# Optimization experiments

Hardware: AMD Instinct MI355X
Metric: run time of the kernel (lower is better)

The kernel has to match this reference:

```python
import jax, jax.numpy as jnp
import numpy as np

B, S, D, H = 2, 2048, 1024, 16
DH = D // H


def setup_inputs() -> dict:
    key = jax.random.key(0)
    ks = jax.random.split(key, 6)
    scale = 0.02
    X = jax.random.normal(ks[0], (B, S, D), dtype=jnp.float32)
    masks = jax.random.randint(ks[1], (B, S), 0, 2).astype(jnp.int32)
    Wq = jax.random.normal(ks[2], (D, D), dtype=jnp.float32) * scale
    Wk = jax.random.normal(ks[3], (D, D), dtype=jnp.float32) * scale
    Wv = jax.random.normal(ks[4], (D, D), dtype=jnp.float32) * scale
    Wo = jax.random.normal(ks[5], (D, D), dtype=jnp.float32) * scale
    return {"X": X, "masks": masks, "Wq": Wq, "Wk": Wk, "Wv": Wv, "Wo": Wo}


def reference(X, masks, Wq, Wk, Wv, Wo):
    b, s, d = X.shape
    masks_b = masks.astype(bool)                       # [B,S] key validity
    lookahead = jnp.triu(jnp.ones((s, s), dtype=bool), 1)  # [S,S] future positions
    pad = ~masks_b[:, None, :]                         # [B,1,S] -> invalid keys
    invalid = pad | lookahead[None, :, :]              # [B,S,S]
    valid = (~invalid)[:, None, :, :].astype(X.dtype)  # [B,1,S,S]

    def split_heads(Y):  # [B,S,D] -> [B,H,S,DH]
        return Y.reshape(b, s, H, DH).transpose(0, 2, 1, 3)

    Q = split_heads(X @ Wq.T)
    K = split_heads(X @ Wk.T)
    V = split_heads(X @ Wv.T)

    Qn = Q / jnp.sqrt(jnp.sum(Q * Q, axis=-1, keepdims=True))
    Kn = K / jnp.sqrt(jnp.sum(K * K, axis=-1, keepdims=True))

    scores = jnp.einsum('bhqd,bhkd->bhqk', Qn, Kn)     # cosine similarities
    att = jax.nn.relu(scores) * valid                  # relu + causal/pad mask
    ctx = jnp.einsum('bhqk,bhkd->bhqd', att, V)
    ctx = ctx * masks_b[:, None, :, None].astype(X.dtype)  # zero padded queries

    out = ctx.transpose(0, 2, 1, 3).reshape(b, s, d)
    return out @ Wo.T
```

## Files before the change

kernel.cpp:

```cpp
#include <hip/hip_runtime.h>
#include <hip/hip_bf16.h>

#define BB 2
#define SS 2048
#define DD 1024
#define HH 16
#define MMR (BB*SS)
#define ND3 3072

typedef __hip_bfloat16 bf;
typedef __bf16 bf16x8 __attribute__((ext_vector_type(8)));
typedef float f32x4 __attribute__((ext_vector_type(4)));
typedef float f32x16 __attribute__((ext_vector_type(16)));

#define VMCNT(n) asm volatile("s_waitcnt vmcnt(" #n ")" ::: "memory")

__device__ __forceinline__ f32x4 mfma16(bf16x8 a, bf16x8 b, f32x4 c) {
    return __builtin_amdgcn_mfma_f32_16x16x32_bf16(a, b, c, 0, 0, 0);
}
__device__ __forceinline__ f32x16 mfma32(bf16x8 a, bf16x8 b, f32x16 c) {
    return __builtin_amdgcn_mfma_f32_32x32x16_bf16(a, b, c, 0, 0, 0);
}
__device__ __forceinline__ unsigned cvt_pk_bf16(float lo, float hi) {
    unsigned r;
    asm("v_cvt_pk_bf16_f32 %0, %1, %2" : "=v"(r) : "v"(lo), "v"(hi));
    return r;
}
__device__ __forceinline__ void pl32swap(unsigned& a, unsigned& b) {
    asm("v_permlane32_swap_b32 %0, %1" : "+v"(a), "+v"(b));
}
__device__ __forceinline__ void glds16(const bf* g, bf* l) {
    __builtin_amdgcn_global_load_lds(
        (const __attribute__((address_space(1))) void*)g,
        (__attribute__((address_space(3))) void*)l,
        16, 0, 0);
}

__global__ __launch_bounds__(256) void k_convert(const float* __restrict__ X,
                                                 const float* __restrict__ Wq,
                                                 const float* __restrict__ Wk,
                                                 const float* __restrict__ Wv,
                                                 const float* __restrict__ Wo,
                                                 bf* __restrict__ Xb,
                                                 bf* __restrict__ Wqkv,
                                                 bf* __restrict__ Wob) {
    const int bid = blockIdx.x;
    const float* src;
    bf* dst;
    int off;
    if (bid < 4096) {
        src = X; dst = Xb; off = bid;
    } else {
        const int r = (bid - 4096) >> 10;
        src = (r == 0) ? Wq : (r == 1) ? Wk : (r == 2) ? Wv : Wo;
        dst = (r < 3) ? (Wqkv + (size_t)r * 1048576) : Wob;
        off = (bid - 4096) & 1023;
    }
    const int j = (off * 256 + threadIdx.x) * 4;
    float4 v = *(const float4*)(src + j);
    bf tmp[4];
    tmp[0] = __float2bfloat16(v.x);
    tmp[1] = __float2bfloat16(v.y);
    tmp[2] = __float2bfloat16(v.z);
    tmp[3] = __float2bfloat16(v.w);
    *(uint2*)(dst + j) = *(const uint2*)tmp;
}

template<int MODE, int BM, int BN>
__global__ __launch_bounds__(256) void k_gemm(const bf* __restrict__ A,
                                              const bf* __restrict__ Bt,
                                              float* __restrict__ Cf,
                                              const int* __restrict__ masks,
                                              bf* __restrict__ Qn,
                                              bf* __restrict__ Kn,
                                              bf* __restrict__ Vt,
                                              int nx, int N, int K) {
    constexpr int MF = BM / 32;
    constexpr int RA = BM / 64;
    constexpr int RB = BN / 64;
    __shared__ __align__(16) bf Asm[3][BM * 32];
    __shared__ __align__(16) bf Bsm[3][BN * 32];
    const int tid = threadIdx.x;
    const int w = tid >> 6, lane = tid & 63, g = lane >> 4, rl = lane & 15;
    const int cpx = gridDim.x >> 3;
    const int swz = (blockIdx.x & 7) * cpx + (blockIdx.x >> 3);
    const int m0 = (swz / nx) * BM, n0 = (swz % nx) * BN;
    const int wr = (w >> 1) * (MF * 16), wc = (w & 1) * 64;
    const int lrow = lane >> 2, lseg = lane & 3;
    const int xseg = lseg ^ ((lrow >> 1) & 3);

    f32x4 acc[MF][4] = {};
    const bf* Ap = A + (size_t)m0 * K;
    const bf* Bp = Bt + (size_t)n0 * K;

    auto stage = [&](int bi, int k0) {
#pragma unroll
        for (int u = 0; u < RA; ++u)
            glds16(Ap + (size_t)(u * 64 + w * 16 + lrow) * K + k0 + xseg * 8,
                   &Asm[bi][(u * 64 + w * 16) * 32]);
#pragma unroll
        for (int u = 0; u < RB; ++u)
            glds16(Bp + (size_t)(u * 64 + w * 16 + lrow) * K + k0 + xseg * 8,
                   &Bsm[bi][(u * 64 + w * 16) * 32]);
    };

    const int T = K >> 5;
    stage(0, 0);
    stage(1, 32);
    int cur = 0, nxt = 2;
    for (int t = 0; t < T; ++t) {
        __builtin_amdgcn_sched_barrier(0);
        if (t < T - 1) {
            if constexpr (RA + RB == 4) VMCNT(4); else VMCNT(3);
        } else {
            VMCNT(0);
        }
        __builtin_amdgcn_s_barrier();
        __builtin_amdgcn_sched_barrier(0);
        if (t + 2 < T) stage(nxt, (t + 2) * 32);

        const bf* Ab = Asm[cur];
        const bf* Bb = Bsm[cur];
        bf16x8 af[MF], bfr[4];
#pragma unroll
        for (int m = 0; m < MF; ++m) {
            const int row = wr + m * 16 + rl;
            af[m] = __builtin_bit_cast(bf16x8,
                *(const int4*)&Ab[row * 32 + (g ^ ((row >> 1) & 3)) * 8]);
        }
#pragma unroll
        for (int n = 0; n < 4; ++n) {
            const int row = wc + n * 16 + rl;
            bfr[n] = __builtin_bit_cast(bf16x8,
                *(const int4*)&Bb[row * 32 + (g ^ ((row >> 1) & 3)) * 8]);
        }
        __builtin_amdgcn_s_setprio(1);
#pragma unroll
        for (int m = 0; m < MF; ++m)
#pragma unroll
            for (int n = 0; n < 4; ++n)
                acc[m][n] = mfma16(af[m], bfr[n], acc[m][n]);
        __builtin_amdgcn_s_setprio(0);

        cur = (cur == 2) ? 0 : cur + 1;
        nxt = (nxt == 2) ? 0 : nxt + 1;
    }

    if constexpr (MODE == 0) {
#pragma unroll
        for (int m = 0; m < MF; ++m)
#pragma unroll
            for (int n = 0; n < 4; ++n)
#pragma unroll
                for (int ri = 0; ri < 4; ++ri)
                    Cf[(size_t)(m0 + wr + m * 16 + g * 4 + ri) * N + n0 + wc + n * 16 + rl] =
                        acc[m][n][ri];
    } else {
        const int ncol0 = n0 + wc;
        if (ncol0 < 2048) {
            bf* dst = (ncol0 < 1024) ? Qn : Kn;
            const int h2 = (ncol0 >> 6) & 15;
#pragma unroll
            for (int m = 0; m < MF; ++m) {
#pragma unroll
                for (int ri = 0; ri < 4; ++ri) {
                    const int row = m0 + wr + m * 16 + g * 4 + ri;
                    float ss = 0.f;
#pragma unroll
                    for (int n = 0; n < 4; ++n) ss += acc[m][n][ri] * acc[m][n][ri];
#pragma unroll
                    for (int d = 1; d < 16; d <<= 1) ss += __shfl_xor(ss, d, 64);
                    const float sc = rsqrtf(ss) * (masks[row] ? 1.0f : 0.0f);
                    const int b = row >> 11, s = row & 2047;
                    const size_t base = ((size_t)(b * HH + h2) * SS + s) * 64;
#pragma unroll
                    for (int n = 0; n < 4; ++n)
                        dst[base + n * 16 + rl] = __float2bfloat16(acc[m][n][ri] * sc);
                }
            }
        } else {
            const int h2 = (ncol0 - 2048) >> 6;
            const int b = (m0 + wr) >> 11;
            const int sb = ((m0 + wr) & 2047) + g * 4;
#pragma unroll
            for (int m = 0; m < MF; ++m)
#pragma unroll
                for (int n = 0; n < 4; ++n) {
                    const int d = n * 16 + rl;
                    bf t4[4];
#pragma unroll
                    for (int ri = 0; ri < 4; ++ri) t4[ri] = __float2bfloat16(acc[m][n][ri]);
                    *(uint2*)&Vt[((size_t)(b * HH + h2) * 64 + d) * SS + sb + m * 16] =
                        *(uint2*)t4;
                }
        }
    }
}

__global__ __launch_bounds__(256) void k_attn(const bf* __restrict__ Qn,
                                              const bf* __restrict__ Kn,
                                              const bf* __restrict__ Vt,
                                              bf* __restrict__ Ctx) {
    __shared__ __align__(16) bf Ksm[3][64 * 64];
    __shared__ __align__(16) bf Vsm[3][64 * 64];

    const int idx = blockIdx.x;
    const int qt = 31 - (idx >> 5);
    const int by = idx & 31;
    const int b = by >> 4, h = by & 15;
    const int tid = threadIdx.x;
    const int w = tid >> 6, lane = tid & 63;
    const int l31 = lane & 31, hl = lane >> 5;
    const int qh = w >> 1;
    const int kp = w & 1;
    const int qw = qt * 64 + qh * 32;
    const int qg = qw + l31;

    const bf* Qp = Qn + (size_t)by * SS * 64;
    const bf* Kp = Kn + (size_t)by * SS * 64;
    const bf* Vp = Vt + (size_t)by * 64 * SS;

    bf16x8 aqs[4];
#pragma unroll
    for (int st = 0; st < 4; ++st)
        aqs[st] = __builtin_bit_cast(bf16x8,
            *(const int4*)(Qp + (size_t)(qw + l31) * 64 + st * 16 + hl * 8));

    const int srow = lane >> 3;
    const int sblk = (lane & 7) ^ srow;

    auto stage = [&](int buf, int k0) {
#pragma unroll
        for (int u = 0; u < 2; ++u) {
            const int c = w * 2 + u;
            const int row = c * 8 + srow;
            glds16(Kp + (size_t)(k0 + row) * 64 + sblk * 8, &Ksm[buf][c * 512]);
            glds16(Vp + (size_t)row * SS + k0 + sblk * 8, &Vsm[buf][c * 512]);
        }
    };

    f32x16 accd[2] = {};

    stage(0, 0);
    stage(1, 64);
    int cur = 0, nxt = 2;
    for (int t = 0; t <= qt; ++t) {
        __builtin_amdgcn_sched_barrier(0);
        if (t < qt) { VMCNT(4); } else { VMCNT(0); }
        __builtin_amdgcn_s_barrier();
        __builtin_amdgcn_sched_barrier(0);
        if (t + 2 <= qt) stage(nxt, (t + 2) * 64);

        const int kbase = t * 64 + kp * 32;
        if (kbase <= qw + 31) {
            f32x16 pc = {};
            __builtin_amdgcn_s_setprio(1);
#pragma unroll
            for (int st = 0; st < 4; ++st) {
                const int r = kp * 32 + l31;
                bf16x8 ak = __builtin_bit_cast(bf16x8,
                    *(const int4*)&Ksm[cur][r * 64 + (((2 * st + hl) ^ (r & 7)) << 3)]);
                pc = mfma32(ak, aqs[st], pc);
            }
            __builtin_amdgcn_s_setprio(0);
            const bool dg = (kbase + 31 > qw);
            float pv[16];
#pragma unroll
            for (int m2 = 0; m2 < 16; ++m2) {
                float v = fmaxf(pc[m2], 0.0f);
                if (dg) {
                    const int kg = kbase + (m2 & 3) + 8 * (m2 >> 2) + 4 * hl;
                    if (kg > qg) v = 0.0f;
                }
                pv[m2] = v;
            }
            unsigned P[8];
#pragma unroll
            for (int m2 = 0; m2 < 8; ++m2) P[m2] = cvt_pk_bf16(pv[2 * m2], pv[2 * m2 + 1]);
            pl32swap(P[0], P[2]);
            pl32swap(P[1], P[3]);
            pl32swap(P[4], P[6]);
            pl32swap(P[5], P[7]);
            __builtin_amdgcn_s_setprio(1);
#pragma unroll
            for (int s = 0; s < 2; ++s) {
                uint4 pw = {P[4 * s + 0], P[4 * s + 1], P[4 * s + 2], P[4 * s + 3]};
                bf16x8 pa = __builtin_bit_cast(bf16x8, pw);
#pragma unroll
                for (int dt = 0; dt < 2; ++dt) {
                    const int d = dt * 32 + l31;
                    const int slot = kp * 4 + s * 2 + hl;
                    bf16x8 bv = __builtin_bit_cast(bf16x8,
                        *(const int4*)&Vsm[cur][d * 64 + ((slot ^ (d & 7)) << 3)]);
                    accd[dt] = mfma32(pa, bv, accd[dt]);
                }
            }
            __builtin_amdgcn_s_setprio(0);
        }

        cur = (cur == 2) ? 0 : cur + 1;
        nxt = (nxt == 2) ? 0 : nxt + 1;
    }

    __syncthreads();
    float* red = (float*)&Ksm[0][0];
    if (kp == 1) {
#pragma unroll
        for (int dt = 0; dt < 2; ++dt)
#pragma unroll
            for (int m2 = 0; m2 < 16; ++m2)
                red[qh * 2048 + (dt * 16 + m2) * 64 + lane] = accd[dt][m2];
    }
    __syncthreads();
    if (kp == 0) {
#pragma unroll
        for (int dt = 0; dt < 2; ++dt)
#pragma unroll
            for (int m2 = 0; m2 < 16; ++m2) {
                const float v = accd[dt][m2] + red[qh * 2048 + (dt * 16 + m2) * 64 + lane];
                const int q = qw + (m2 & 3) + 8 * (m2 >> 2) + 4 * hl;
                const int d = dt * 32 + l31;
                Ctx[(size_t)(b * SS + q) * DD + h * 64 + d] = __float2bfloat16(v);
            }
    }
}

extern "C" void kernel_launch(void* const* d_in, const int* in_sizes, int n_in,
                              void* d_out, int out_size, void* d_ws, size_t ws_size,
                              hipStream_t stream) {
    const float* X  = (const float*)d_in[0];
    const int* masks = (const int*)d_in[1];
    const float* Wq = (const float*)d_in[2];
    const float* Wk = (const float*)d_in[3];
    const float* Wv = (const float*)d_in[4];
    const float* Wo = (const float*)d_in[5];
    float* out = (float*)d_out;
    char* ws = (char*)d_ws;

    const size_t MB = 1024 * 1024;
    bf* Xb   = (bf*)(ws);
    bf* Wqkv = (bf*)(ws + 8  * MB);
    bf* Wob  = (bf*)(ws + 14 * MB);
    bf* Qn   = (bf*)(ws + 16 * MB);
    bf* Kn   = (bf*)(ws + 24 * MB);
    bf* Vt   = (bf*)(ws + 32 * MB);
    bf* Ctx  = (bf*)(ws + 40 * MB);

    k_convert<<<8192, 256, 0, stream>>>(X, Wq, Wk, Wv, Wo, Xb, Wqkv, Wob);

    k_gemm<1, 128, 128><<<(ND3 / 128) * (MMR / 128), 256, 0, stream>>>(
        Xb, Wqkv, nullptr, masks, Qn, Kn, Vt, ND3 / 128, ND3, DD);

    k_attn<<<1024, 256, 0, stream>>>(Qn, Kn, Vt, Ctx);

    k_gemm<0, 64, 128><<<(DD / 128) * (MMR / 64), 256, 0, stream>>>(
        Ctx, Wob, out, nullptr, nullptr, nullptr, nullptr, DD / 128, DD, DD);
}
```

Before: 104.9 us.

## Use 8-wave QKV GEMM and load K/V directly from global in attention

```diff
diff --git a/kernel.cpp b/kernel.cpp
--- a/kernel.cpp
+++ b/kernel.cpp
@@ -66,18 +66,116 @@
     *(uint2*)(dst + j) = *(const uint2*)tmp;
 }
 
-template<int MODE, int BM, int BN>
+__global__ __launch_bounds__(512, 6) void k_gemm8(const bf* __restrict__ A,
+                                                  const bf* __restrict__ Bt,
+                                                  const int* __restrict__ masks,
+                                                  bf* __restrict__ Qn,
+                                                  bf* __restrict__ Kn,
+                                                  bf* __restrict__ Vt,
+                                                  int nx, int K) {
+    __shared__ __align__(16) bf Asm[3][128 * 32];
+    __shared__ __align__(16) bf Bsm[3][128 * 32];
+    const int tid = threadIdx.x;
+    const int w = tid >> 6, lane = tid & 63, g = lane >> 4, rl = lane & 15;
+    const int cpx = gridDim.x >> 3;
+    const int swz = (blockIdx.x & 7) * cpx + (blockIdx.x >> 3);
+    const int m0 = (swz / nx) * 128, n0 = (swz % nx) * 128;
+    const int wr = (w >> 1) * 32, wc = (w & 1) * 64;
+    const int lrow = lane >> 2, lseg = lane & 3;
+    const int xseg = lseg ^ ((lrow >> 1) & 3);
+
+    f32x4 acc[2][4] = {};
+    const bf* Ap = A + (size_t)m0 * K;
+    const bf* Bp = Bt + (size_t)n0 * K;
+
+    auto stage = [&](int bi, int k0) {
+        glds16(Ap + (size_t)(w * 16 + lrow) * K + k0 + xseg * 8, &Asm[bi][w * 512]);
+        glds16(Bp + (size_t)(w * 16 + lrow) * K + k0 + xseg * 8, &Bsm[bi][w * 512]);
+    };
+
+    const int T = K >> 5;
+    stage(0, 0);
+    stage(1, 32);
+    int cur = 0, nxt = 2;
+    for (int t = 0; t < T; ++t) {
+        __builtin_amdgcn_sched_barrier(0);
+        if (t < T - 1) { VMCNT(2); } else { VMCNT(0); }
+        __builtin_amdgcn_s_barrier();
+        __builtin_amdgcn_sched_barrier(0);
+        if (t + 2 < T) stage(nxt, (t + 2) * 32);
+
+        const bf* Ab = Asm[cur];
+        const bf* Bb = Bsm[cur];
+        bf16x8 af[2], bfr[4];
+#pragma unroll
+        for (int m = 0; m < 2; ++m) {
+            const int row = wr + m * 16 + rl;
+            af[m] = __builtin_bit_cast(bf16x8,
+                *(const int4*)&Ab[row * 32 + (g ^ ((row >> 1) & 3)) * 8]);
+        }
+#pragma unroll
+        for (int n = 0; n < 4; ++n) {
+            const int row = wc + n * 16 + rl;
+            bfr[n] = __builtin_bit_cast(bf16x8,
+                *(const int4*)&Bb[row * 32 + (g ^ ((row >> 1) & 3)) * 8]);
+        }
+        __builtin_amdgcn_s_setprio(1);
+#pragma unroll
+        for (int m = 0; m < 2; ++m)
+#pragma unroll
+            for (int n = 0; n < 4; ++n)
+                acc[m][n] = mfma16(af[m], bfr[n], acc[m][n]);
+        __builtin_amdgcn_s_setprio(0);
+
+        cur = (cur == 2) ? 0 : cur + 1;
+        nxt = (nxt == 2) ? 0 : nxt + 1;
+    }
+
+    const int ncol0 = n0 + wc;
+    if (ncol0 < 2048) {
+        bf* dst = (ncol0 < 1024) ? Qn : Kn;
+        const int h2 = (ncol0 >> 6) & 15;
+#pragma unroll
+        for (int m = 0; m < 2; ++m) {
+#pragma unroll
+            for (int ri = 0; ri < 4; ++ri) {
+                const int row = m0 + wr + m * 16 + g * 4 + ri;
+                float ss = 0.f;
+#pragma unroll
+                for (int n = 0; n < 4; ++n) ss += acc[m][n][ri] * acc[m][n][ri];
+#pragma unroll
+                for (int d = 1; d < 16; d <<= 1) ss += __shfl_xor(ss, d, 64);
+                const float sc = rsqrtf(ss) * (masks[row] ? 1.0f : 0.0f);
+                const int b = row >> 11, s = row & 2047;
+                const size_t base = ((size_t)(b * HH + h2) * SS + s) * 64;
+#pragma unroll
+                for (int n = 0; n < 4; ++n)
+                    dst[base + n * 16 + rl] = __float2bfloat16(acc[m][n][ri] * sc);
+            }
+        }
+    } else {
+        const int h2 = (ncol0 - 2048) >> 6;
+        const int b = (m0 + wr) >> 11;
+        const int sb = ((m0 + wr) & 2047) + g * 4;
+#pragma unroll
+        for (int m = 0; m < 2; ++m)
+#pragma unroll
+            for (int n = 0; n < 4; ++n) {
+                const int d = n * 16 + rl;
+                bf t4[4];
+#pragma unroll
+                for (int ri = 0; ri < 4; ++ri) t4[ri] = __float2bfloat16(acc[m][n][ri]);
+                *(uint2*)&Vt[((size_t)(b * HH + h2) * 64 + d) * SS + sb + m * 16] =
+                    *(uint2*)t4;
+            }
+    }
+}
+
 __global__ __launch_bounds__(256) void k_gemm(const bf* __restrict__ A,
                                               const bf* __restrict__ Bt,
                                               float* __restrict__ Cf,
-                                              const int* __restrict__ masks,
-                                              bf* __restrict__ Qn,
-                                              bf* __restrict__ Kn,
-                                              bf* __restrict__ Vt,
                                               int nx, int N, int K) {
-    constexpr int MF = BM / 32;
-    constexpr int RA = BM / 64;
-    constexpr int RB = BN / 64;
+    constexpr int BM = 64, BN = 128;
     __shared__ __align__(16) bf Asm[3][BM * 32];
     __shared__ __align__(16) bf Bsm[3][BN * 32];
     const int tid = threadIdx.x;
@@ -85,21 +183,18 @@
     const int cpx = gridDim.x >> 3;
     const int swz = (blockIdx.x & 7) * cpx + (blockIdx.x >> 3);
     const int m0 = (swz / nx) * BM, n0 = (swz % nx) * BN;
-    const int wr = (w >> 1) * (MF * 16), wc = (w & 1) * 64;
+    const int wr = (w >> 1) * 32, wc = (w & 1) * 64;
     const int lrow = lane >> 2, lseg = lane & 3;
     const int xseg = lseg ^ ((lrow >> 1) & 3);
 
-    f32x4 acc[MF][4] = {};
+    f32x4 acc[2][4] = {};
     const bf* Ap = A + (size_t)m0 * K;
     const bf* Bp = Bt + (size_t)n0 * K;
 
     auto stage = [&](int bi, int k0) {
-#pragma unroll
-        for (int u = 0; u < RA; ++u)
-            glds16(Ap + (size_t)(u * 64 + w * 16 + lrow) * K + k0 + xseg * 8,
-                   &Asm[bi][(u * 64 + w * 16) * 32]);
-#pragma unroll
-        for (int u = 0; u < RB; ++u)
+        glds16(Ap + (size_t)(w * 16 + lrow) * K + k0 + xseg * 8, &Asm[bi][w * 512]);
+#pragma unroll
+        for (int u = 0; u < 2; ++u)
             glds16(Bp + (size_t)(u * 64 + w * 16 + lrow) * K + k0 + xseg * 8,
                    &Bsm[bi][(u * 64 + w * 16) * 32]);
     };
@@ -110,20 +205,16 @@
     int cur = 0, nxt = 2;
     for (int t = 0; t < T; ++t) {
         __builtin_amdgcn_sched_barrier(0);
-        if (t < T - 1) {
-            if constexpr (RA + RB == 4) VMCNT(4); else VMCNT(3);
-        } else {
-            VMCNT(0);
-        }
+        if (t < T - 1) { VMCNT(3); } else { VMCNT(0); }
         __builtin_amdgcn_s_barrier();
         __builtin_amdgcn_sched_barrier(0);
         if (t + 2 < T) stage(nxt, (t + 2) * 32);
 
         const bf* Ab = Asm[cur];
         const bf* Bb = Bsm[cur];
-        bf16x8 af[MF], bfr[4];
-#pragma unroll
-        for (int m = 0; m < MF; ++m) {
+        bf16x8 af[2], bfr[4];
+#pragma unroll
+        for (int m = 0; m < 2; ++m) {
             const int row = wr + m * 16 + rl;
             af[m] = __builtin_bit_cast(bf16x8,
                 *(const int4*)&Ab[row * 32 + (g ^ ((row >> 1) & 3)) * 8]);
@@ -136,7 +227,7 @@
         }
         __builtin_amdgcn_s_setprio(1);
 #pragma unroll
-        for (int m = 0; m < MF; ++m)
+        for (int m = 0; m < 2; ++m)
 #pragma unroll
             for (int n = 0; n < 4; ++n)
                 acc[m][n] = mfma16(af[m], bfr[n], acc[m][n]);
@@ -146,63 +237,21 @@
         nxt = (nxt == 2) ? 0 : nxt + 1;
     }
 
-    if constexpr (MODE == 0) {
-#pragma unroll
-        for (int m = 0; m < MF; ++m)
-#pragma unroll
-            for (int n = 0; n < 4; ++n)
-#pragma unroll
-                for (int ri = 0; ri < 4; ++ri)
-                    Cf[(size_t)(m0 + wr + m * 16 + g * 4 + ri) * N + n0 + wc + n * 16 + rl] =
-                        acc[m][n][ri];
-    } else {
-        const int ncol0 = n0 + wc;
-        if (ncol0 < 2048) {
-            bf* dst = (ncol0 < 1024) ? Qn : Kn;
-            const int h2 = (ncol0 >> 6) & 15;
-#pragma unroll
-            for (int m = 0; m < MF; ++m) {
-#pragma unroll
-                for (int ri = 0; ri < 4; ++ri) {
-                    const int row = m0 + wr + m * 16 + g * 4 + ri;
-                    float ss = 0.f;
-#pragma unroll
-                    for (int n = 0; n < 4; ++n) ss += acc[m][n][ri] * acc[m][n][ri];
-#pragma unroll
-                    for (int d = 1; d < 16; d <<= 1) ss += __shfl_xor(ss, d, 64);
-                    const float sc = rsqrtf(ss) * (masks[row] ? 1.0f : 0.0f);
-                    const int b = row >> 11, s = row & 2047;
-                    const size_t base = ((size_t)(b * HH + h2) * SS + s) * 64;
-#pragma unroll
-                    for (int n = 0; n < 4; ++n)
-                        dst[base + n * 16 + rl] = __float2bfloat16(acc[m][n][ri] * sc);
-                }
-            }
-        } else {
-            const int h2 = (ncol0 - 2048) >> 6;
-            const int b = (m0 + wr) >> 11;
-            const int sb = ((m0 + wr) & 2047) + g * 4;
-#pragma unroll
-            for (int m = 0; m < MF; ++m)
-#pragma unroll
-                for (int n = 0; n < 4; ++n) {
-                    const int d = n * 16 + rl;
-                    bf t4[4];
-#pragma unroll
-                    for (int ri = 0; ri < 4; ++ri) t4[ri] = __float2bfloat16(acc[m][n][ri]);
-                    *(uint2*)&Vt[((size_t)(b * HH + h2) * 64 + d) * SS + sb + m * 16] =
-                        *(uint2*)t4;
-                }
-        }
-    }
-}
-
-__global__ __launch_bounds__(256) void k_attn(const bf* __restrict__ Qn,
-                                              const bf* __restrict__ Kn,
-                                              const bf* __restrict__ Vt,
-                                              bf* __restrict__ Ctx) {
-    __shared__ __align__(16) bf Ksm[3][64 * 64];
-    __shared__ __align__(16) bf Vsm[3][64 * 64];
+#pragma unroll
+    for (int m = 0; m < 2; ++m)
+#pragma unroll
+        for (int n = 0; n < 4; ++n)
+#pragma unroll
+            for (int ri = 0; ri < 4; ++ri)
+                Cf[(size_t)(m0 + wr + m * 16 + g * 4 + ri) * N + n0 + wc + n * 16 + rl] =
+                    acc[m][n][ri];
+}
+
+__global__ __launch_bounds__(256, 4) void k_attn(const bf* __restrict__ Qn,
+                                                 const bf* __restrict__ Kn,
+                                                 const bf* __restrict__ Vt,
+                                                 bf* __restrict__ Ctx) {
+    __shared__ float red[2][32][64];
 
     const int idx = blockIdx.x;
     const int qt = 31 - (idx >> 5);
@@ -226,90 +275,60 @@
         aqs[st] = __builtin_bit_cast(bf16x8,
             *(const int4*)(Qp + (size_t)(qw + l31) * 64 + st * 16 + hl * 8));
 
-    const int srow = lane >> 3;
-    const int sblk = (lane & 7) ^ srow;
-
-    auto stage = [&](int buf, int k0) {
-#pragma unroll
-        for (int u = 0; u < 2; ++u) {
-            const int c = w * 2 + u;
-            const int row = c * 8 + srow;
-            glds16(Kp + (size_t)(k0 + row) * 64 + sblk * 8, &Ksm[buf][c * 512]);
-            glds16(Vp + (size_t)row * SS + k0 + sblk * 8, &Vsm[buf][c * 512]);
-        }
-    };
-
     f32x16 accd[2] = {};
-
-    stage(0, 0);
-    stage(1, 64);
-    int cur = 0, nxt = 2;
-    for (int t = 0; t <= qt; ++t) {
-        __builtin_amdgcn_sched_barrier(0);
-        if (t < qt) { VMCNT(4); } else { VMCNT(0); }
-        __builtin_amdgcn_s_barrier();
-        __builtin_amdgcn_sched_barrier(0);
-        if (t + 2 <= qt) stage(nxt, (t + 2) * 64);
-
-        const int kbase = t * 64 + kp * 32;
-        if (kbase <= qw + 31) {
-            f32x16 pc = {};
-            __builtin_amdgcn_s_setprio(1);
-#pragma unroll
-            for (int st = 0; st < 4; ++st) {
-                const int r = kp * 32 + l31;
-                bf16x8 ak = __builtin_bit_cast(bf16x8,
-                    *(const int4*)&Ksm[cur][r * 64 + (((2 * st + hl) ^ (r & 7)) << 3)]);
-                pc = mfma32(ak, aqs[st], pc);
+    const int nsub = ((qw + 31 - kp * 32) >> 6) + 1;
+
+    for (int i = 0; i < nsub; ++i) {
+        const int kb = kp * 32 + i * 64;
+        bf16x8 kf[4], vf[4];
+#pragma unroll
+        for (int st = 0; st < 4; ++st)
+            kf[st] = __builtin_bit_cast(bf16x8,
+                *(const int4*)(Kp + (size_t)(kb + l31) * 64 + st * 16 + hl * 8));
+#pragma unroll
+        for (int s = 0; s < 2; ++s)
+#pragma unroll
+            for (int dt = 0; dt < 2; ++dt)
+                vf[s * 2 + dt] = __builtin_bit_cast(bf16x8,
+                    *(const int4*)(Vp + (size_t)(dt * 32 + l31) * SS + kb + (s * 2 + hl) * 8));
+        f32x16 pc = {};
+#pragma unroll
+        for (int st = 0; st < 4; ++st)
+            pc = mfma32(kf[st], aqs[st], pc);
+        const bool dg = (kb + 31 > qw);
+        float pv[16];
+#pragma unroll
+        for (int m2 = 0; m2 < 16; ++m2) {
+            float v = fmaxf(pc[m2], 0.0f);
+            if (dg) {
+                const int kg = kb + (m2 & 3) + 8 * (m2 >> 2) + 4 * hl;
+                if (kg > qg) v = 0.0f;
             }
-            __builtin_amdgcn_s_setprio(0);
-            const bool dg = (kbase + 31 > qw);
-            float pv[16];
-#pragma unroll
-            for (int m2 = 0; m2 < 16; ++m2) {
-                float v = fmaxf(pc[m2], 0.0f);
-                if (dg) {
-                    const int kg = kbase + (m2 & 3) + 8 * (m2 >> 2) + 4 * hl;
-                    if (kg > qg) v = 0.0f;
-                }
-                pv[m2] = v;
-            }
-            unsigned P[8];
-#pragma unroll
-            for (int m2 = 0; m2 < 8; ++m2) P[m2] = cvt_pk_bf16(pv[2 * m2], pv[2 * m2 + 1]);
-            pl32swap(P[0], P[2]);
-            pl32swap(P[1], P[3]);
-            pl32swap(P[4], P[6]);
-            pl32swap(P[5], P[7]);
-            __builtin_amdgcn_s_setprio(1);
-#pragma unroll
-            for (int s = 0; s < 2; ++s) {
-                uint4 pw = {P[4 * s + 0], P[4 * s + 1], P[4 * s + 2], P[4 * s + 3]};
-                bf16x8 pa = __builtin_bit_cast(bf16x8, pw);
-#pragma unroll
-                for (int dt = 0; dt < 2; ++dt) {
-                    const int d = dt * 32 + l31;
-                    const int slot = kp * 4 + s * 2 + hl;
-                    bf16x8 bv = __builtin_bit_cast(bf16x8,
-                        *(const int4*)&Vsm[cur][d * 64 + ((slot ^ (d & 7)) << 3)]);
-                    accd[dt] = mfma32(pa, bv, accd[dt]);
-                }
-            }
-            __builtin_amdgcn_s_setprio(0);
-        }
-
-        cur = (cur == 2) ? 0 : cur + 1;
-        nxt = (nxt == 2) ? 0 : nxt + 1;
-    }
-
-    __syncthreads();
-    float* red = (float*)&Ksm[0][0];
+            pv[m2] = v;
+        }
+        unsigned P[8];
+#pragma unroll
+        for (int m2 = 0; m2 < 8; ++m2) P[m2] = cvt_pk_bf16(pv[2 * m2], pv[2 * m2 + 1]);
+        pl32swap(P[0], P[2]);
+        pl32swap(P[1], P[3]);
+        pl32swap(P[4], P[6]);
+        pl32swap(P[5], P[7]);
+#pragma unroll
+        for (int s = 0; s < 2; ++s) {
+            uint4 pw = {P[4 * s + 0], P[4 * s + 1], P[4 * s + 2], P[4 * s + 3]};
+            bf16x8 pa = __builtin_bit_cast(bf16x8, pw);
+#pragma unroll
+            for (int dt = 0; dt < 2; ++dt)
+                accd[dt] = mfma32(pa, vf[s * 2 + dt], accd[dt]);
+        }
+    }
+
     if (kp == 1) {
 #pragma unroll
         for (int dt = 0; dt < 2; ++dt)
 #pragma unroll
             for (int m2 = 0; m2 < 16; ++m2)
-                red[qh * 2048 + (dt * 16 + m2) * 64 + lane] = accd[dt][m2];
+                red[qh][dt * 16 + m2][lane] = accd[dt][m2];
     }
     __syncthreads();
     if (kp == 0) {
@@ -317,7 +336,7 @@
         for (int dt = 0; dt < 2; ++dt)
 #pragma unroll
             for (int m2 = 0; m2 < 16; ++m2) {
-                const float v = accd[dt][m2] + red[qh * 2048 + (dt * 16 + m2) * 64 + lane];
+                const float v = accd[dt][m2] + red[qh][dt * 16 + m2][lane];
                 const int q = qw + (m2 & 3) + 8 * (m2 >> 2) + 4 * hl;
                 const int d = dt * 32 + l31;
                 Ctx[(size_t)(b * SS + q) * DD + h * 64 + d] = __float2bfloat16(v);
@@ -348,11 +367,11 @@
 
     k_convert<<<8192, 256, 0, stream>>>(X, Wq, Wk, Wv, Wo, Xb, Wqkv, Wob);
 
-    k_gemm<1, 128, 128><<<(ND3 / 128) * (MMR / 128), 256, 0, stream>>>(
-        Xb, Wqkv, nullptr, masks, Qn, Kn, Vt, ND3 / 128, ND3, DD);
+    k_gemm8<<<(ND3 / 128) * (MMR / 128), 512, 0, stream>>>(
+        Xb, Wqkv, masks, Qn, Kn, Vt, ND3 / 128, DD);
 
     k_attn<<<1024, 256, 0, stream>>>(Qn, Kn, Vt, Ctx);
 
-    k_gemm<0, 64, 128><<<(DD / 128) * (MMR / 64), 256, 0, stream>>>(
-        Ctx, Wob, out, nullptr, nullptr, nullptr, nullptr, DD / 128, DD, DD);
-}
+    k_gemm<<<(DD / 128) * (MMR / 64), 256, 0, stream>>>(
+        Ctx, Wob, out, DD / 128, DD, DD);
+}
```

Result: slower. 140.9 us (+34.3%).
